# Performance work log

Hardware: AMD Instinct MI355X
Metric: run time of the kernel (lower is better)

## Reference

```python
import jax, jax.numpy as jnp
import numpy as np
import math

B, L, D_MODEL = 2, 2048, 1024
D_KEY = 128
M = 32768          # samg_nodes, graph assumed full (n_active == M)
TOP_K = 32
N_HOPS = 3
EDGE_MAX = 8
SURPRISE_TEMP = 0.1
EPS = 1e-8


def setup_inputs() -> dict:
    key = jax.random.key(0)
    ks = jax.random.split(key, 10)
    h = jax.random.normal(ks[0], (B, L, D_MODEL), dtype=jnp.float32)
    W_q = jax.random.normal(ks[1], (D_KEY, D_MODEL), dtype=jnp.float32) * 0.02
    W_k = jax.random.normal(ks[2], (D_KEY, D_MODEL), dtype=jnp.float32) * 0.02
    W_v = jax.random.normal(ks[3], (D_MODEL, D_MODEL), dtype=jnp.float32) * 0.02
    W_mu_w = jax.random.normal(ks[4], (D_MODEL, 2 * D_MODEL), dtype=jnp.float32) * 0.02
    W_mu_b = jnp.zeros((D_MODEL,), dtype=jnp.float32)
    node_keys = jax.random.normal(ks[5], (M, D_KEY), dtype=jnp.float32)
    node_values = jax.random.normal(ks[6], (M, D_MODEL), dtype=jnp.float32)
    node_edges = jax.random.randint(ks[7], (M, EDGE_MAX), 0, M, dtype=jnp.int32)
    edge_weights = jax.random.uniform(ks[8], (M, EDGE_MAX), dtype=jnp.float32)
    surprise_tau = jnp.asarray(1.0, dtype=jnp.float32)
    return {"h": h, "W_q": W_q, "W_k": W_k, "W_v": W_v,
            "W_mu_w": W_mu_w, "W_mu_b": W_mu_b,
            "node_keys": node_keys, "node_values": node_values,
            "edge_weights": edge_weights, "surprise_tau": surprise_tau,
            "node_edges": node_edges}


def _normalize(x, axis=-1):
    return x / jnp.sqrt(jnp.sum(x * x, axis=axis, keepdims=True) + 1e-12)


def _read(h, W_q, node_keys, node_values, node_edges, edge_weights):
    # SAMG.read with n_active == M
    q = jnp.einsum('bld,kd->blk', h, W_q)           # [B,L,d_key]
    q_norm = _normalize(q)
    k_norm = _normalize(node_keys)                   # rows unit-norm -> gathers stay normalized
    scores = jnp.einsum('bld,nd->bln', q_norm, k_norm)   # [B,L,M]
    topk_scores, topk_idx = jax.lax.top_k(scores, TOP_K)
    scale = math.sqrt(D_KEY)
    for _hop in range(N_HOPS - 1):
        nb_idx = node_edges[topk_idx]                # [B,L,K,E]
        nb_w = edge_weights[topk_idx]                # [B,L,K,E]
        valid = (nb_idx >= 0) & (nb_idx < M)
        flat_idx = jnp.clip(nb_idx, 0, M - 1)
        nb_keys = k_norm[flat_idx]                   # [B,L,K,E,d_key] (already normalized)
        sim = jnp.einsum('bld,blked->blke', q_norm, nb_keys)
        hop_scores = sim * nb_w * valid.astype(sim.dtype)
        all_scores = jnp.concatenate([topk_scores, hop_scores.reshape(*hop_scores.shape[:2], -1)], axis=-1)
        all_idx = jnp.concatenate([topk_idx, flat_idx.reshape(*flat_idx.shape[:2], -1)], axis=-1)
        topk_scores, sel = jax.lax.top_k(all_scores, TOP_K)
        topk_idx = jnp.take_along_axis(all_idx, sel, axis=-1)
    alpha = jax.nn.softmax(topk_scores / scale, axis=-1)   # [B,L,K]
    r = jnp.einsum('blk,blkd->bld', alpha, node_values[topk_idx])
    return r


def reference(h, W_q, W_k, W_v, W_mu_w, W_mu_b,
              node_keys, node_values, edge_weights, surprise_tau, node_edges):
    v = jnp.einsum('bld,od->blo', h, W_v)                 # [B,L,d_model]
    r = _read(h, W_q, node_keys, node_values, node_edges, edge_weights)
    # surprise gate: normalized prediction error
    diff_sq = jnp.sum((v - r) ** 2, axis=-1)
    norm_sq = jnp.sum(v * v, axis=-1) + EPS
    surprise = diff_sq / norm_sq
    gate = jax.nn.sigmoid((surprise - surprise_tau) / SURPRISE_TEMP)  # [B,L]
    # fuse retrieved memory with h (W_mu over [h; r]), gated residual
    fused = jnp.einsum('blc,oc->blo', jnp.concatenate([h, r], axis=-1), W_mu_w) + W_mu_b
    h_mem = h + gate[..., None] * fused
    return h_mem


if __name__ == '__main__':
    out = reference(**setup_inputs())
    print(out.shape, out.dtype)
```

## Files before the change

### kernel.cpp

```cpp
#include <hip/hip_runtime.h>
#include <cstdint>
#include <cmath>

#define NQ 4096
#define DM 1024
#define DK 128
#define MN 32768
#define TK 32
#define EM 8
#define NSPLIT 64
#define SPN (MN/NSPLIT)
#define QT 128
#define CAP 512
#define SLOTS 8
#define OCAP 1024
#define TAU 0.24f

typedef __attribute__((ext_vector_type(8))) short short8v;
typedef __attribute__((ext_vector_type(4))) float f32x4;

__device__ __forceinline__ bool better_pair(float av, int ai, float bv, int bi) {
  return (av > bv) || (av == bv && ai < bi);
}

__device__ __forceinline__ short f2bf(float x) {
  unsigned u = __builtin_bit_cast(unsigned, x);
  unsigned r = (u + 0x7fffu + ((u >> 16) & 1u)) >> 16;
  return (short)r;
}
__device__ __forceinline__ float bf2f(short s) {
  return __builtin_bit_cast(float, ((unsigned)(unsigned short)s) << 16);
}

__device__ __forceinline__ void load_lds16(const short* g, short* l) {
  __builtin_amdgcn_global_load_lds(
      (const __attribute__((address_space(1))) unsigned*)g,
      (__attribute__((address_space(3))) unsigned*)l, 16, 0, 0);
}

__device__ __forceinline__ int swz(int row, int d) {
  return (d & ~63) | (((((d >> 3) & 7) ^ (row & 7))) << 3) | (d & 7);
}

__global__ __launch_bounds__(256) void k_keys(const float* __restrict__ keys,
                                              float* __restrict__ knorm,
                                              short* __restrict__ kb) {
  __shared__ float rows[64][DK + 1];
  __shared__ float rinv[64];
  const int tid = threadIdx.x;
  const int r0 = blockIdx.x * 64;
  for (int j = 0; j < 8; ++j) {
    int e = tid + 256 * j;
    int r = e >> 5;
    int c = (e & 31) * 4;
    float4 v = *(const float4*)(keys + (size_t)(r0 + r) * DK + c);
    rows[r][c + 0] = v.x; rows[r][c + 1] = v.y;
    rows[r][c + 2] = v.z; rows[r][c + 3] = v.w;
  }
  __syncthreads();
  if (tid < 64) {
    float ss = 0.f;
    #pragma unroll 4
    for (int d = 0; d < DK; ++d) { float x = rows[tid][d]; ss += x * x; }
    rinv[tid] = 1.0f / sqrtf(ss + 1e-12f);
  }
  __syncthreads();
  for (int j = 0; j < 32; ++j) {
    int e = tid + 256 * j;
    int r = e >> 7;
    int d = e & 127;
    float x = rows[r][d] * rinv[r];
    const int gr = r0 + r;
    knorm[(size_t)gr * DK + d] = x;
    const int ph = ((d >> 3) ^ (gr & 7));
    kb[(size_t)gr * DK + ph * 8 + (d & 7)] = f2bf(x);
  }
}

__global__ __launch_bounds__(256) void k_tobf16s(const float* __restrict__ src,
                                                 short* __restrict__ dst,
                                                 int n4, int krow) {
  const int stride = gridDim.x * 256;
  for (int i = blockIdx.x * 256 + threadIdx.x; i < n4; i += stride) {
    float4 v = ((const float4*)src)[i];
    short4 o;
    o.x = f2bf(v.x); o.y = f2bf(v.y); o.z = f2bf(v.z); o.w = f2bf(v.w);
    const int d = i * 4;
    const int row = d / krow;
    const int dr = d - row * krow;
    *(short4*)(dst + (size_t)row * krow + swz(row, dr)) = o;
  }
}

__global__ __launch_bounds__(64) void k_qnorm2(const float* __restrict__ qraw,
                                               float* __restrict__ qn,
                                               short* __restrict__ qb,
                                               int* __restrict__ ocnt) {
  const int q = blockIdx.x;
  const int lane = threadIdx.x;
  if (q == 0 && lane == 0) ocnt[0] = 0;
  float2 v = *(const float2*)(qraw + (size_t)q * DK + lane * 2);
  float ss = v.x * v.x + v.y * v.y;
  #pragma unroll
  for (int off = 32; off; off >>= 1) ss += __shfl_xor(ss, off);
  const float rinv = 1.0f / sqrtf(ss + 1e-12f);
  const float ax = v.x * rinv, ay = v.y * rinv;
  *(float2*)(qn + (size_t)q * DK + lane * 2) = make_float2(ax, ay);
  short2 o; o.x = f2bf(ax); o.y = f2bf(ay);
  *(short2*)(qb + (size_t)q * DK + lane * 2) = o;
}

__global__ __launch_bounds__(256) void k_screen(
    const short* __restrict__ qb, const short* __restrict__ kb,
    int2* __restrict__ pairs, int4* __restrict__ oflow, int* __restrict__ ocnt) {
  __shared__ int cnt[QT];
  __shared__ int2 cand[QT][SLOTS];
  __shared__ short tiles[2][16 * DK];
  const int tid = threadIdx.x;
  const int lane = tid & 63;
  const int w = tid >> 6;
  const int qg = blockIdx.x >> 6;
  const int sp = blockIdx.x & (NSPLIT - 1);
  const int q0 = qg * QT + w * 32;
  const int n0s = sp * SPN;
  const int lrow = lane & 15;
  const int sent = __float_as_int(-1e30f);
  const int lkof = (lane >> 4) << 3;

  for (int i = tid; i < QT * SLOTS; i += 256)
    ((int2*)cand)[i] = make_int2(sent, 0x7fffffff);
  if (tid < QT) cnt[tid] = 0;

  short8v a[2][4];
  #pragma unroll
  for (int qt = 0; qt < 2; ++qt)
    #pragma unroll
    for (int s = 0; s < 4; ++s)
      a[qt][s] = *(const short8v*)(qb + (((size_t)(q0 + qt * 16 + lrow)) << 7) + s * 32 + lkof);

  load_lds16(kb + (((size_t)n0s) << 7) + (w << 9) + (lane << 3),
             &tiles[0][(w << 9) + (lane << 3)]);
  __syncthreads();

  int buf = 0;
  for (int nt = 0; nt < SPN / 16; ++nt) {
    if (nt + 1 < SPN / 16)
      load_lds16(kb + (((size_t)(n0s + (nt + 1) * 16)) << 7) + (w << 9) + (lane << 3),
                 &tiles[buf ^ 1][(w << 9) + (lane << 3)]);
    const int n0 = n0s + nt * 16;
    const int n = n0 + lrow;
    short8v bA[4];
    #pragma unroll
    for (int s = 0; s < 4; ++s) {
      const int ph = (s * 4 + (lane >> 4)) ^ (lrow & 7);
      bA[s] = *(const short8v*)&tiles[buf][lrow * DK + ph * 8];
    }
    #pragma unroll
    for (int qt = 0; qt < 2; ++qt) {
      f32x4 acc = {0.f, 0.f, 0.f, 0.f};
      #pragma unroll
      for (int s = 0; s < 4; ++s)
        acc = __builtin_amdgcn_mfma_f32_16x16x32_bf16(a[qt][s], bA[s], acc, 0, 0, 0);
      #pragma unroll
      for (int rg = 0; rg < 4; ++rg) {
        if (acc[rg] > TAU) {
          const int ql = w * 32 + qt * 16 + ((lane >> 4) << 2) + rg;
          const int slot = atomicAdd(&cnt[ql], 1);
          if (slot < SLOTS) {
            cand[ql][slot] = make_int2(__float_as_int(acc[rg]), n);
          } else {
            const int os = atomicAdd(ocnt, 1);
            if (os < OCAP)
              oflow[os] = make_int4(qg * QT + ql, __float_as_int(acc[rg]), n, 0);
          }
        }
      }
    }
    __syncthreads();
    buf ^= 1;
  }
  const int ql2 = w * 32 + (lane >> 1);
  const int half = (lane & 1) * 4;
  const size_t gbase = ((size_t)(qg * QT + ql2) * NSPLIT + sp) * SLOTS + half;
  *(int4*)&pairs[gbase]     = *(const int4*)&cand[ql2][half];
  *(int4*)&pairs[gbase + 2] = *(const int4*)&cand[ql2][half + 2];
}

__global__ __launch_bounds__(256) void k_select(
    const int2* __restrict__ pairs, const int4* __restrict__ oflow, const int* __restrict__ ocnt,
    const float* __restrict__ qn, const float* __restrict__ knorm,
    float* __restrict__ tv, int* __restrict__ ti) {
  __shared__ float qs[4][DK];
  const int tid = threadIdx.x;
  const int lane = tid & 63;
  const int w = tid >> 6;
  const int q = blockIdx.x * 4 + w;
  for (int i = tid; i < 4 * DK; i += 256)
    qs[i >> 7][i & 127] = qn[(size_t)(blockIdx.x * 4 + (i >> 7)) * DK + (i & 127)];
  __syncthreads();
  float v[8]; int ix[8];
  const int2* pp = pairs + (size_t)q * CAP;
  #pragma unroll
  for (int t = 0; t < 8; ++t) {
    const int2 pr = pp[lane + t * 64];
    v[t] = __int_as_float(pr.x);
    ix[t] = pr.y;
  }
  int nof = ocnt[0]; if (nof > OCAP) nof = OCAP;
  for (int i = 0; i < nof; ++i) {
    const int4 e = oflow[i];
    if (e.x == q) {
      float mv = v[0]; int mt = 0;
      #pragma unroll
      for (int t = 1; t < 8; ++t) if (v[t] < mv) { mv = v[t]; mt = t; }
      int mli = (lane << 3) | mt;
      #pragma unroll
      for (int off = 32; off; off >>= 1) {
        const float o = __shfl_xor(mv, off); const int ol = __shfl_xor(mli, off);
        if (o < mv || (o == mv && ol < mli)) { mv = o; mli = ol; }
      }
      const int wl = mli >> 3, wt = mli & 7;
      if (lane == wl) {
        #pragma unroll
        for (int t = 0; t < 8; ++t) if (t == wt) { v[t] = __int_as_float(e.y); ix[t] = e.z; }
      }
    }
  }
  #pragma unroll
  for (int k = 2; k <= 512; k <<= 1) {
    #pragma unroll
    for (int j = k >> 1; j; j >>= 1) {
      if (j >= 64) {
        const int tb = j >> 6;
        #pragma unroll
        for (int t = 0; t < 8; ++t) {
          if ((t & tb) == 0) {
            const int t2 = t + tb;
            const bool dir = (((t * 64) & k) == 0);
            const bool pb = better_pair(v[t2], ix[t2], v[t], ix[t]);
            if (pb == dir) {
              float tvv = v[t]; v[t] = v[t2]; v[t2] = tvv;
              int tii = ix[t]; ix[t] = ix[t2]; ix[t2] = tii;
            }
          }
        }
      } else {
        #pragma unroll
        for (int t = 0; t < 8; ++t) {
          const float ov = __shfl_xor(v[t], j);
          const int oi = __shfl_xor(ix[t], j);
          const bool lower = (lane & j) == 0;
          const bool dir = (((t * 64 + lane) & k) == 0);
          const bool pb = better_pair(ov, oi, v[t], ix[t]);
          if ((pb == lower) == dir) { v[t] = ov; ix[t] = oi; }
        }
      }
    }
  }
  const int ci = ix[0];
  const bool valid = (unsigned)ci < (unsigned)MN;
  const int cc = valid ? ci : 0;
  float dot = 0.f;
  const float4* kp = (const float4*)(knorm + (size_t)cc * DK);
  const float4* qp = (const float4*)&qs[w][0];
  #pragma unroll 8
  for (int i = 0; i < DK / 4; ++i) {
    const float4 kv = kp[i];
    const float4 qv = qp[i];
    dot += qv.x * kv.x + qv.y * kv.y + qv.z * kv.z + qv.w * kv.w;
  }
  float dv = valid ? dot : -1e30f;
  int di = valid ? ci : 0x7fffffff;
  #pragma unroll
  for (int k = 2; k <= 64; k <<= 1) {
    #pragma unroll
    for (int j = k >> 1; j; j >>= 1) {
      const float ov = __shfl_xor(dv, j);
      const int oi = __shfl_xor(di, j);
      const bool lower = (lane & j) == 0;
      const bool dirdesc = (lane & k) == 0;
      const bool pb = better_pair(ov, oi, dv, di);
      if ((pb == lower) == dirdesc) { dv = ov; di = oi; }
    }
  }
  if (lane < TK) {
    tv[(size_t)q * TK + lane] = dv;
    ti[(size_t)q * TK + lane] = di;
  }
}

__global__ __launch_bounds__(256) void k_hops_sel(
    const float* __restrict__ qn, const float* __restrict__ knorm,
    const short* __restrict__ kb,
    const int* __restrict__ edges, const float* __restrict__ ew,
    const float* __restrict__ tval, const int* __restrict__ tidx,
    float* __restrict__ aout, int* __restrict__ iout) {
  __shared__ float qs[DK];
  __shared__ float cval[TK]; __shared__ int cidx[TK];
  __shared__ float av[TK + EM * TK]; __shared__ int ai[TK + EM * TK];
  __shared__ int   p1[TK];
  __shared__ float sc1[TK * EM];
  __shared__ int   nb1[TK * EM];
  const int tid = threadIdx.x;
  const int q = blockIdx.x;
  if (tid < DK) qs[tid] = qn[(size_t)q * DK + tid];
  if (tid < TK) { cval[tid] = tval[(size_t)q * TK + tid]; cidx[tid] = tidx[(size_t)q * TK + tid]; }
  __syncthreads();
  for (int hop = 0; hop < 2; ++hop) {
    const int k = tid >> 3, e = tid & 7;
    int parent = cidx[k];
    parent = parent < 0 ? 0 : (parent >= MN ? MN - 1 : parent);
    const float floor32 = cval[TK - 1];
    float sc; int nbc;
    int hit = -1;
    if (hop == 1) {
      for (int j = 0; j < TK; ++j)
        if (p1[j] == parent) { hit = j; break; }
    }
    if (hit >= 0) {
      sc = sc1[hit * EM + e];
      nbc = nb1[hit * EM + e];
    } else {
      const int nb = edges[(size_t)parent * EM + e];
      const float wgt = ew[(size_t)parent * EM + e];
      const bool valid = (nb >= 0) && (nb < MN);
      nbc = nb < 0 ? 0 : (nb >= MN ? MN - 1 : nb);
      if (!valid || wgt <= floor32 * 0.999f) {
        sc = 0.0f;
      } else {
        float d0a = 0.f, d1a = 0.f, d2a = 0.f, d3a = 0.f;
        const short8v* kr = (const short8v*)(kb + (size_t)nbc * DK);
        const int rx = nbc & 7;
        #pragma unroll
        for (int s = 0; s < 8; ++s) {
          const short8v k0 = kr[(s * 2 + 0) ^ rx];
          const short8v k1 = kr[(s * 2 + 1) ^ rx];
          #pragma unroll
          for (int u = 0; u < 4; ++u) {
            d0a += qs[(s * 2 + 0) * 8 + u] * bf2f(k0[u]);
            d1a += qs[(s * 2 + 0) * 8 + 4 + u] * bf2f(k0[4 + u]);
            d2a += qs[(s * 2 + 1) * 8 + u] * bf2f(k1[u]);
            d3a += qs[(s * 2 + 1) * 8 + 4 + u] * bf2f(k1[4 + u]);
          }
        }
        const float sca = ((d0a + d1a) + (d2a + d3a)) * wgt;
        if (sca <= floor32 - 2e-3f) {
          sc = sca;
        } else {
          float4 a0 = make_float4(0.f, 0.f, 0.f, 0.f);
          float4 a1 = make_float4(0.f, 0.f, 0.f, 0.f);
          const float4* kp = (const float4*)(knorm + (size_t)nbc * DK);
          const float4* qp = (const float4*)&qs[0];
          #pragma unroll
          for (int i = 0; i < 16; ++i) {
            const float4 k0 = kp[i * 2 + 0], q0 = qp[i * 2 + 0];
            const float4 k1 = kp[i * 2 + 1], q1 = qp[i * 2 + 1];
            a0.x += q0.x * k0.x; a0.y += q0.y * k0.y; a0.z += q0.z * k0.z; a0.w += q0.w * k0.w;
            a1.x += q1.x * k1.x; a1.y += q1.y * k1.y; a1.z += q1.z * k1.z; a1.w += q1.w * k1.w;
          }
          const float dot = (a0.x + a0.y + a0.z + a0.w) + (a1.x + a1.y + a1.z + a1.w);
          sc = dot * wgt;
        }
      }
    }
    if (hop == 0) {
      if (e == 0) p1[k] = parent;
      sc1[tid] = sc; nb1[tid] = nbc;
    }
    const int ndisp = __syncthreads_count(sc > floor32);
    if (ndisp == 0) {
      if (hop == 0) break;
      continue;
    }
    if (tid < TK) { av[tid] = cval[tid]; ai[tid] = cidx[tid]; }
    av[TK + tid] = sc; ai[TK + tid] = nbc;
    __syncthreads();
    if (tid < 64) {
      float sv[5];
      #pragma unroll
      for (int t = 0; t < 5; ++t) { const int p = tid + t * 64; sv[t] = (p < 288) ? av[p] : -1e30f; }
      for (int rr = 0; rr < TK; ++rr) {
        float bv = -1e30f; int bp = 1 << 30;
        #pragma unroll
        for (int t = 0; t < 5; ++t) { const int p = tid + t * 64; if (sv[t] > bv) { bv = sv[t]; bp = p; } }
        #pragma unroll
        for (int off = 32; off; off >>= 1) {
          const float ov = __shfl_xor(bv, off); const int op = __shfl_xor(bp, off);
          if (ov > bv || (ov == bv && op < bp)) { bv = ov; bp = op; }
        }
        if (tid == 0) { cval[rr] = bv; cidx[rr] = ai[bp]; }
        #pragma unroll
        for (int t = 0; t < 5; ++t) { if (tid + t * 64 == bp) sv[t] = -1e30f; }
      }
    }
    __syncthreads();
  }
  if (tid < 64) {
    const float s = (tid < TK) ? cval[tid] / 11.313708498984761f : -1e30f;
    float m = s;
    #pragma unroll
    for (int off = 32; off; off >>= 1) m = fmaxf(m, __shfl_xor(m, off));
    const float ex = (tid < TK) ? expf(s - m) : 0.f;
    float sum = ex;
    #pragma unroll
    for (int off = 32; off; off >>= 1) sum += __shfl_xor(sum, off);
    if (tid < TK) {
      aout[(size_t)q * TK + tid] = ex / sum;
      iout[(size_t)q * TK + tid] = cidx[tid];
    }
  }
}

template <int BF16V>
__global__ __launch_bounds__(256) void k_rgather(
    const float* __restrict__ ain, const int* __restrict__ iin,
    const float* __restrict__ vals, const short* __restrict__ nvb,
    short* __restrict__ rbb) {
  __shared__ float alpha[TK];
  __shared__ int cidx[TK];
  const int q = blockIdx.x;
  const int tid = threadIdx.x;
  if (tid < TK) {
    alpha[tid] = ain[(size_t)q * TK + tid];
    cidx[tid] = iin[(size_t)q * TK + tid];
  }
  __syncthreads();
  const int d0 = tid * 4;
  float ox = 0, oy = 0, oz = 0, ow = 0;
  if (BF16V) {
    #pragma unroll
    for (int g = 0; g < 4; ++g) {
      short4 vr[8];
      #pragma unroll
      for (int j = 0; j < 8; ++j)
        vr[j] = *(const short4*)(nvb + (size_t)cidx[g * 8 + j] * DM + d0);
      #pragma unroll
      for (int j = 0; j < 8; ++j) {
        const float a = alpha[g * 8 + j];
        ox += a * bf2f(vr[j].x); oy += a * bf2f(vr[j].y);
        oz += a * bf2f(vr[j].z); ow += a * bf2f(vr[j].w);
      }
    }
  } else {
    #pragma unroll 4
    for (int kk = 0; kk < TK; ++kk) {
      const float a = alpha[kk];
      const float4 vv = *(const float4*)(vals + (size_t)cidx[kk] * DM + d0);
      ox += a * vv.x; oy += a * vv.y; oz += a * vv.z; ow += a * vv.w;
    }
  }
  short4 o16;
  o16.x = f2bf(ox); o16.y = f2bf(oy); o16.z = f2bf(oz); o16.w = f2bf(ow);
  *(short4*)(rbb + (size_t)q * DM + swz(q, d0)) = o16;
}

__global__ __launch_bounds__(256) void k_gemm(
    const float* __restrict__ A0, const float* __restrict__ W,
    const float* __restrict__ bias, float* __restrict__ C, int K, int ldc) {
  __shared__ float As[16][64];
  __shared__ float Bs[16][64];
  const int tid = threadIdx.x;
  const int tm = tid >> 4, tn = tid & 15;
  const int row0 = blockIdx.y * 64, col0 = blockIdx.x * 64;
  float4 acc[4];
  #pragma unroll
  for (int i = 0; i < 4; ++i) acc[i] = make_float4(0.f, 0.f, 0.f, 0.f);
  const int lr = tid >> 2;
  const int lk = (tid & 3) * 4;
  for (int kt = 0; kt < K; kt += 16) {
    const int gk = kt + lk;
    float4 a4 = *(const float4*)(A0 + (size_t)(row0 + lr) * K + gk);
    As[lk + 0][lr] = a4.x; As[lk + 1][lr] = a4.y; As[lk + 2][lr] = a4.z; As[lk + 3][lr] = a4.w;
    float4 b4 = *(const float4*)(W + (size_t)(col0 + lr) * K + gk);
    Bs[lk + 0][lr] = b4.x; Bs[lk + 1][lr] = b4.y; Bs[lk + 2][lr] = b4.z; Bs[lk + 3][lr] = b4.w;
    __syncthreads();
    #pragma unroll
    for (int kk = 0; kk < 16; ++kk) {
      const float4 a = *(const float4*)&As[kk][tm * 4];
      const float4 b = *(const float4*)&Bs[kk][tn * 4];
      acc[0].x += a.x * b.x; acc[0].y += a.x * b.y; acc[0].z += a.x * b.z; acc[0].w += a.x * b.w;
      acc[1].x += a.y * b.x; acc[1].y += a.y * b.y; acc[1].z += a.y * b.z; acc[1].w += a.y * b.w;
      acc[2].x += a.z * b.x; acc[2].y += a.z * b.y; acc[2].z += a.z * b.z; acc[2].w += a.z * b.w;
      acc[3].x += a.w * b.x; acc[3].y += a.w * b.y; acc[3].z += a.w * b.z; acc[3].w += a.w * b.w;
    }
    __syncthreads();
  }
  float4 b4 = make_float4(0.f, 0.f, 0.f, 0.f);
  if (bias) b4 = *(const float4*)(bias + col0 + tn * 4);
  #pragma unroll
  for (int i = 0; i < 4; ++i) {
    const int row = row0 + tm * 4 + i;
    float4 o = acc[i];
    o.x += b4.x; o.y += b4.y; o.z += b4.z; o.w += b4.w;
    *(float4*)(C + (size_t)row * ldc + col0 + tn * 4) = o;
  }
}

__global__ __launch_bounds__(512) void k_bgemm(
    const short* __restrict__ A0, const short* __restrict__ A1, int KA0,
    const short* __restrict__ B, const float* __restrict__ bias,
    float* __restrict__ C, int K) {
  __shared__ short At[2][128 * 64];
  __shared__ short Bt[2][128 * 64];
  const int tid = threadIdx.x;
  const int lane = tid & 63;
  const int w = tid >> 6;
  const int wm = w & 3, wn = w >> 2;
  const int bid = blockIdx.x;
  const int xcd = bid & 7;
  const int sl = bid >> 3;
  const int mblk = xcd * 4 + (sl & 3);
  const int nblk = sl >> 2;
  const int m0 = mblk * 128;
  const int n0 = nblk * 128;
  const int lm = wm * 32, ln = wn * 64;
  const int lrow = lane & 15;
  f32x4 acc[2][4];
  #pragma unroll
  for (int mi = 0; mi < 2; ++mi)
    #pragma unroll
    for (int ni = 0; ni < 4; ++ni) acc[mi][ni] = (f32x4){0.f, 0.f, 0.f, 0.f};

  #define BG_STAGE(bf, k0_)                                                        \
    {                                                                              \
      const short* Ab_ = ((k0_) < KA0) ? A0 : A1;                                  \
      const int kk_ = ((k0_) < KA0) ? (k0_) : ((k0_) - KA0);                       \
      _Pragma("unroll")                                                            \
      for (int i = 0; i < 2; ++i) {                                                \
        const int eo = (w * 2 + i) * 512 + lane * 8;                               \
        const int r = eo >> 6, ce = eo & 63;                                       \
        load_lds16(Ab_ + (size_t)(m0 + r) * KA0 + kk_ + ce, &At[bf][eo]);          \
        load_lds16(B + (size_t)(n0 + r) * K + (k0_) + ce, &Bt[bf][eo]);            \
      }                                                                            \
    }

  BG_STAGE(0, 0);
  __syncthreads();
  for (int k0 = 0; k0 < K; k0 += 64) {
    const int bf = (k0 >> 6) & 1;
    if (k0 + 64 < K) BG_STAGE(bf ^ 1, k0 + 64);
    short8v fa[2][2], fb[4][2];
    #pragma unroll
    for (int mi = 0; mi < 2; ++mi) {
      const int r = lm + mi * 16 + lrow;
      #pragma unroll
      for (int hf = 0; hf < 2; ++hf) {
        const int ph = (hf * 4 + (lane >> 4)) ^ (r & 7);
        fa[mi][hf] = *(const short8v*)&At[bf][r * 64 + ph * 8];
      }
    }
    #pragma unroll
    for (int ni = 0; ni < 4; ++ni) {
      const int r = ln + ni * 16 + lrow;
      #pragma unroll
      for (int hf = 0; hf < 2; ++hf) {
        const int ph = (hf * 4 + (lane >> 4)) ^ (r & 7);
        fb[ni][hf] = *(const short8v*)&Bt[bf][r * 64 + ph * 8];
      }
    }
    #pragma unroll
    for (int hf = 0; hf < 2; ++hf)
      #pragma unroll
      for (int mi = 0; mi < 2; ++mi)
        #pragma unroll
        for (int ni = 0; ni < 4; ++ni)
          acc[mi][ni] = __builtin_amdgcn_mfma_f32_16x16x32_bf16(fa[mi][hf], fb[ni][hf],
                                                                acc[mi][ni], 0, 0, 0);
    __syncthreads();
  }
  const int rbase = (lane >> 4) << 2;
  #pragma unroll
  for (int mi = 0; mi < 2; ++mi)
    #pragma unroll
    for (int ni = 0; ni < 4; ++ni) {
      const int col = n0 + ln + ni * 16 + lrow;
      const float badd = bias ? bias[col] : 0.f;
      #pragma unroll
      for (int rg = 0; rg < 4; ++rg) {
        const int row = m0 + lm + mi * 16 + rbase + rg;
        C[(size_t)row * DM + col] = acc[mi][ni][rg] + badd;
      }
    }
}

__global__ __launch_bounds__(256) void k_epi(
    const float* __restrict__ h, const short* __restrict__ rbb,
    const float* __restrict__ v, const float* __restrict__ fu,
    const float* __restrict__ tau_p, float* __restrict__ out) {
  __shared__ float red[8];
  __shared__ float sgate;
  const int q = blockIdx.x;
  const int tid = threadIdx.x;
  const size_t base = (size_t)q * DM + tid * 4;
  const float4 vv = *(const float4*)(v + base);
  const short4 r4 = *(const short4*)(rbb + (size_t)q * DM + swz(q, tid * 4));
  const float rx = bf2f(r4.x), ry = bf2f(r4.y), rz = bf2f(r4.z), rw = bf2f(r4.w);
  const float dx = vv.x - rx, dy = vv.y - ry, dz = vv.z - rz, dw = vv.w - rw;
  float ds = dx * dx + dy * dy + dz * dz + dw * dw;
  float vs = vv.x * vv.x + vv.y * vv.y + vv.z * vv.z + vv.w * vv.w;
  #pragma unroll
  for (int off = 32; off; off >>= 1) { ds += __shfl_xor(ds, off); vs += __shfl_xor(vs, off); }
  const int wv = tid >> 6;
  if ((tid & 63) == 0) { red[wv * 2] = ds; red[wv * 2 + 1] = vs; }
  __syncthreads();
  if (tid == 0) {
    const float DS = red[0] + red[2] + red[4] + red[6];
    const float VS = red[1] + red[3] + red[5] + red[7];
    const float sur = DS / (VS + 1e-8f);
    const float g = (sur - tau_p[0]) / 0.1f;
    sgate = 1.f / (1.f + expf(-g));
  }
  __syncthreads();
  const float gt = sgate;
  const float4 hh = *(const float4*)(h + base);
  const float4 ff = *(const float4*)(fu + base);
  float4 o;
  o.x = hh.x + gt * ff.x; o.y = hh.y + gt * ff.y;
  o.z = hh.z + gt * ff.z; o.w = hh.w + gt * ff.w;
  *(float4*)(out + base) = o;
}

extern "C" void kernel_launch(void* const* d_in, const int* in_sizes, int n_in,
                              void* d_out, int out_size, void* d_ws, size_t ws_size,
                              hipStream_t stream) {
  const float* h   = (const float*)d_in[0];
  const float* Wq  = (const float*)d_in[1];
  const float* Wv  = (const float*)d_in[3];
  const float* Wmu = (const float*)d_in[4];
  const float* Wmb = (const float*)d_in[5];
  const float* nk  = (const float*)d_in[6];
  const float* nv  = (const float*)d_in[7];
  const float* ew  = (const float*)d_in[8];
  const float* tau = (const float*)d_in[9];
  const int*   ne  = (const int*)d_in[10];
  float* out = (float*)d_out;

  char* base = (char*)d_ws;
  float* knorm = (float*)(base);
  float* fb    = (float*)(base + (32ull << 20));
  short* kb    = (short*)(base + (16ull << 20));
  short* qb    = (short*)(base + (24ull << 20));
  int2*  pairs = (int2*) (base + (25ull << 20));
  float* qn    = (float*)(base + (41ull << 20));
  int4*  oflow = (int4*) (base + (43ull << 20));
  int*   ocnt  = (int*)  (base + (43ull << 20) + 16384);
  float* tv    = (float*)(base + (44ull << 20));
  int*   ti    = (int*)  (base + (45ull << 20));
  float* qraw  = (float*)(base + (46ull << 20));
  float* aw    = (float*)(base + (46ull << 20));
  int*   ci    = (int*)  (base + (47ull << 20));
  short* hb    = (short*)(base + (48ull << 20));
  short* Wvb   = (short*)(base + (56ull << 20));
  short* Wmub  = (short*)(base + (58ull << 20));
  short* rbb   = (short*)(base + (62ull << 20));
  short* nvb   = (short*)(base + (70ull << 20));
  float* vb    = (float*)(base);

  const bool bf16v = ws_size >= (134ull << 20);

  k_keys<<<MN / 64, 256, 0, stream>>>(nk, knorm, kb);
  k_tobf16s<<<1024, 256, 0, stream>>>(h,   hb,   NQ * DM / 4, DM);
  k_tobf16s<<<512,  256, 0, stream>>>(Wv,  Wvb,  DM * DM / 4, DM);
  k_tobf16s<<<1024, 256, 0, stream>>>(Wmu, Wmub, DM * 2 * DM / 4, 2 * DM);
  if (bf16v)
    k_tobf16s<<<2048, 256, 0, stream>>>(nv, nvb, MN * DM / 4, 1 << 30);
  dim3 gq(DK / 64, NQ / 64);
  k_gemm<<<gq, 256, 0, stream>>>(h, Wq, (const float*)nullptr, qraw, DM, DK);
  k_qnorm2<<<NQ, 64, 0, stream>>>(qraw, qn, qb, ocnt);
  k_screen<<<(NQ / QT) * NSPLIT, 256, 0, stream>>>(qb, kb, pairs, oflow, ocnt);
  k_select<<<NQ / 4, 256, 0, stream>>>(pairs, oflow, ocnt, qn, knorm, tv, ti);
  k_hops_sel<<<NQ, 256, 0, stream>>>(qn, knorm, kb, ne, ew, tv, ti, aw, ci);
  if (bf16v)
    k_rgather<1><<<NQ, 256, 0, stream>>>(aw, ci, nv, nvb, rbb);
  else
    k_rgather<0><<<NQ, 256, 0, stream>>>(aw, ci, nv, nvb, rbb);
  k_bgemm<<<256, 512, 0, stream>>>(hb, (const short*)nullptr, DM, Wvb,
                                   (const float*)nullptr, vb, DM);
  k_bgemm<<<256, 512, 0, stream>>>(hb, rbb, DM, Wmub, Wmb, fb, 2 * DM);
  k_epi<<<NQ, 256, 0, stream>>>(h, rbb, vb, fb, tau, out);
}
```

Baseline: 417.3 us.

## Split neighbor bf16 dot products across 4 lanes and drop hop-1 parent cache

The neighbor-scoring loop in the hop kernel now has each group of 4 lanes share one bf16 key row, reading 16-byte chunks in a coalesced pattern and reducing with shuffles, over 4 passes covering 256 candidates. The fp32 re-check for near-threshold scores moves to a separate per-thread phase after a barrier. The hop-1 reuse of hop-0 parent scores (shared-memory cache plus linear search) is removed. Each candidate is recomputed instead. The aim is better memory coalescing and less divergence, at the cost of extra passes, shuffles and one more barrier.

After: 407.4 us. 2.4% less time.

```diff
diff --git a/kernel.cpp b/kernel.cpp
--- a/kernel.cpp
+++ b/kernel.cpp
@@ -297,75 +297,65 @@
     float* __restrict__ aout, int* __restrict__ iout) {
   __shared__ float qs[DK];
   __shared__ float cval[TK]; __shared__ int cidx[TK];
+  __shared__ float scs[256]; __shared__ int nbs[256];
   __shared__ float av[TK + EM * TK]; __shared__ int ai[TK + EM * TK];
-  __shared__ int   p1[TK];
-  __shared__ float sc1[TK * EM];
-  __shared__ int   nb1[TK * EM];
   const int tid = threadIdx.x;
   const int q = blockIdx.x;
+  const int grp = tid >> 2, s = tid & 3;
   if (tid < DK) qs[tid] = qn[(size_t)q * DK + tid];
   if (tid < TK) { cval[tid] = tval[(size_t)q * TK + tid]; cidx[tid] = tidx[(size_t)q * TK + tid]; }
   __syncthreads();
   for (int hop = 0; hop < 2; ++hop) {
-    const int k = tid >> 3, e = tid & 7;
-    int parent = cidx[k];
-    parent = parent < 0 ? 0 : (parent >= MN ? MN - 1 : parent);
     const float floor32 = cval[TK - 1];
-    float sc; int nbc;
-    int hit = -1;
-    if (hop == 1) {
-      for (int j = 0; j < TK; ++j)
-        if (p1[j] == parent) { hit = j; break; }
-    }
-    if (hit >= 0) {
-      sc = sc1[hit * EM + e];
-      nbc = nb1[hit * EM + e];
-    } else {
-      const int nb = edges[(size_t)parent * EM + e];
-      const float wgt = ew[(size_t)parent * EM + e];
+    #pragma unroll
+    for (int pass = 0; pass < 4; ++pass) {
+      const int c = pass * 64 + grp;
+      int parent = cidx[c >> 3];
+      parent = parent < 0 ? 0 : (parent >= MN ? MN - 1 : parent);
+      const int nb = edges[(size_t)parent * EM + (c & 7)];
+      const float wgt = ew[(size_t)parent * EM + (c & 7)];
       const bool valid = (nb >= 0) && (nb < MN);
-      nbc = nb < 0 ? 0 : (nb >= MN ? MN - 1 : nb);
-      if (!valid || wgt <= floor32 * 0.999f) {
-        sc = 0.0f;
-      } else {
-        float d0a = 0.f, d1a = 0.f, d2a = 0.f, d3a = 0.f;
+      const int nbc = nb < 0 ? 0 : (nb >= MN ? MN - 1 : nb);
+      const bool live = valid && (wgt > floor32 * 0.999f);
+      float d = 0.f;
+      if (live) {
         const short8v* kr = (const short8v*)(kb + (size_t)nbc * DK);
         const int rx = nbc & 7;
         #pragma unroll
-        for (int s = 0; s < 8; ++s) {
-          const short8v k0 = kr[(s * 2 + 0) ^ rx];
-          const short8v k1 = kr[(s * 2 + 1) ^ rx];
+        for (int j = 0; j < 4; ++j) {
+          const int pc = j * 4 + s;
+          const short8v kv = kr[pc];
+          const int lc = pc ^ rx;
           #pragma unroll
-          for (int u = 0; u < 4; ++u) {
-            d0a += qs[(s * 2 + 0) * 8 + u] * bf2f(k0[u]);
-            d1a += qs[(s * 2 + 0) * 8 + 4 + u] * bf2f(k0[4 + u]);
-            d2a += qs[(s * 2 + 1) * 8 + u] * bf2f(k1[u]);
-            d3a += qs[(s * 2 + 1) * 8 + 4 + u] * bf2f(k1[4 + u]);
-          }
+          for (int u = 0; u < 8; ++u) d += qs[lc * 8 + u] * bf2f(kv[u]);
         }
-        const float sca = ((d0a + d1a) + (d2a + d3a)) * wgt;
-        if (sca <= floor32 - 2e-3f) {
-          sc = sca;
-        } else {
-          float4 a0 = make_float4(0.f, 0.f, 0.f, 0.f);
-          float4 a1 = make_float4(0.f, 0.f, 0.f, 0.f);
-          const float4* kp = (const float4*)(knorm + (size_t)nbc * DK);
-          const float4* qp = (const float4*)&qs[0];
-          #pragma unroll
-          for (int i = 0; i < 16; ++i) {
-            const float4 k0 = kp[i * 2 + 0], q0 = qp[i * 2 + 0];
-            const float4 k1 = kp[i * 2 + 1], q1 = qp[i * 2 + 1];
-            a0.x += q0.x * k0.x; a0.y += q0.y * k0.y; a0.z += q0.z * k0.z; a0.w += q0.w * k0.w;
-            a1.x += q1.x * k1.x; a1.y += q1.y * k1.y; a1.z += q1.z * k1.z; a1.w += q1.w * k1.w;
-          }
-          const float dot = (a0.x + a0.y + a0.z + a0.w) + (a1.x + a1.y + a1.z + a1.w);
-          sc = dot * wgt;
+      }
+      d += __shfl_xor(d, 1);
+      d += __shfl_xor(d, 2);
+      if (s == 0) { scs[c] = live ? d * wgt : 0.0f; nbs[c] = nbc; }
+    }
+    __syncthreads();
+    float sc = scs[tid];
+    {
+      const int c = tid;
+      if (sc > floor32 - 2e-3f) {
+        int parent = cidx[c >> 3];
+        parent = parent < 0 ? 0 : (parent >= MN ? MN - 1 : parent);
+        const float wgt = ew[(size_t)parent * EM + (c & 7)];
+        const int nbc = nbs[c];
+        float4 a0 = make_float4(0.f, 0.f, 0.f, 0.f);
+        float4 a1 = make_float4(0.f, 0.f, 0.f, 0.f);
+        const float4* kp = (const float4*)(knorm + (size_t)nbc * DK);
+        const float4* qp = (const float4*)&qs[0];
+        #pragma unroll
+        for (int i = 0; i < 16; ++i) {
+          const float4 k0 = kp[i * 2 + 0], q0 = qp[i * 2 + 0];
+          const float4 k1 = kp[i * 2 + 1], q1 = qp[i * 2 + 1];
+          a0.x += q0.x * k0.x; a0.y += q0.y * k0.y; a0.z += q0.z * k0.z; a0.w += q0.w * k0.w;
+          a1.x += q1.x * k1.x; a1.y += q1.y * k1.y; a1.z += q1.z * k1.z; a1.w += q1.w * k1.w;
         }
-      }
-    }
-    if (hop == 0) {
-      if (e == 0) p1[k] = parent;
-      sc1[tid] = sc; nb1[tid] = nbc;
+        sc = ((a0.x + a0.y + a0.z + a0.w) + (a1.x + a1.y + a1.z + a1.w)) * wgt;
+      }
     }
     const int ndisp = __syncthreads_count(sc > floor32);
     if (ndisp == 0) {
@@ -373,7 +363,7 @@
       continue;
     }
     if (tid < TK) { av[tid] = cval[tid]; ai[tid] = cidx[tid]; }
-    av[TK + tid] = sc; ai[TK + tid] = nbc;
+    av[TK + tid] = sc; ai[TK + tid] = nbs[tid];
     __syncthreads();
     if (tid < 64) {
       float sv[5];
@@ -396,11 +386,11 @@
     __syncthreads();
   }
   if (tid < 64) {
-    const float s = (tid < TK) ? cval[tid] / 11.313708498984761f : -1e30f;
-    float m = s;
+    const float sx = (tid < TK) ? cval[tid] / 11.313708498984761f : -1e30f;
+    float m = sx;
     #pragma unroll
     for (int off = 32; off; off >>= 1) m = fmaxf(m, __shfl_xor(m, off));
-    const float ex = (tid < TK) ? expf(s - m) : 0.f;
+    const float ex = (tid < TK) ? expf(sx - m) : 0.f;
     float sum = ex;
     #pragma unroll
     for (int off = 32; off; off >>= 1) sum += __shfl_xor(sum, off);
```
